# Performance work log

Hardware: AMD Instinct MI355X
Metric: run time of the kernel (lower is better)

Reference implementation:

```python
import jax, jax.numpy as jnp
import numpy as np

N_CODES = 8192
CODE_DIM = 256


def setup_inputs() -> dict:
    key = jax.random.key(0)
    kx, ke = jax.random.split(key)
    x = jax.random.normal(kx, (16, 4096, CODE_DIM), dtype=jnp.float32)
    # nn.Embedding weight initialized uniform(-1/n, 1/n)
    emb = jax.random.uniform(ke, (N_CODES, CODE_DIM), dtype=jnp.float32,
                             minval=-1.0 / N_CODES, maxval=1.0 / N_CODES)
    return {"x": x, "emb": emb}


def reference(x, emb):
    B, T, D = x.shape
    flat = x.reshape(-1, D)                                   # [BT, D]
    # squared euclidean distance: ||f||^2 - 2 f.e^T + ||e||^2  -> [BT, N]
    dist = ((flat * flat).sum(axis=1, keepdims=True)
            - 2.0 * flat @ emb.T
            + (emb * emb).sum(axis=1))
    idx = jnp.argmin(dist, axis=1)                            # [BT] int
    quant = emb[idx].reshape(x.shape)                         # [B, T, D]
    # commitment-style loss: mse(stop_grad(quant), x)
    loss = jnp.mean(jnp.square(jax.lax.stop_gradient(quant) - x))
    # straight-through estimator
    y = x + jax.lax.stop_gradient(quant - x)
    return y, idx.reshape(B, T), loss
```

## Files before the change

kernel.cpp:

```cpp
#include <hip/hip_runtime.h>
#include <stdint.h>


#define NCODES 8192
#define DDIM   256
#define BT     65536

#define TM     128
#define TN     128
#define NSEG   256
#define F4S    17

#define CAPC   48
#define MARGIN 7e-4f
#define TOKPB  128
#define CCODES 64
#define CHUNKS 128
#define KSCALE 1048576.0f
#define KOFF   131072.0f
#define KMARG  737

typedef float  f32x4  __attribute__((ext_vector_type(4)));
typedef __bf16 bf16x8 __attribute__((ext_vector_type(8)));

#define GLDS16(g, l) __builtin_amdgcn_global_load_lds(                         \
    (const __attribute__((address_space(1))) void*)(g),                        \
    (__attribute__((address_space(3))) void*)(l), 16, 0, 0)
#define GLDS4(g, l) __builtin_amdgcn_global_load_lds(                          \
    (const __attribute__((address_space(1))) void*)(g),                        \
    (__attribute__((address_space(3))) void*)(l), 4, 0, 0)

__device__ __forceinline__ unsigned int fenc(float f) {
  unsigned int u = __float_as_uint(f);
  return (u & 0x80000000u) ? ~u : (u | 0x80000000u);
}
__device__ __forceinline__ float fdec(unsigned int u) {
  unsigned int v = (u & 0x80000000u) ? (u ^ 0x80000000u) : ~u;
  return __uint_as_float(v);
}

__device__ __forceinline__ float np_pairwise256_sq(const float4* __restrict__ row) {
#pragma clang fp contract(off)
  float half[2];
  #pragma unroll
  for (int h = 0; h < 2; h++) {
    float r0,r1,r2,r3,r4,r5,r6,r7;
    float4 q0 = row[h*32 + 0];
    float4 q1 = row[h*32 + 1];
    r0 = q0.x*q0.x; r1 = q0.y*q0.y; r2 = q0.z*q0.z; r3 = q0.w*q0.w;
    r4 = q1.x*q1.x; r5 = q1.y*q1.y; r6 = q1.z*q1.z; r7 = q1.w*q1.w;
    #pragma unroll
    for (int g = 1; g < 16; g++) {
      q0 = row[h*32 + g*2];
      q1 = row[h*32 + g*2 + 1];
      r0 += q0.x*q0.x; r1 += q0.y*q0.y; r2 += q0.z*q0.z; r3 += q0.w*q0.w;
      r4 += q1.x*q1.x; r5 += q1.y*q1.y; r6 += q1.z*q1.z; r7 += q1.w*q1.w;
    }
    half[h] = ((r0+r1) + (r2+r3)) + ((r4+r5) + (r6+r7));
  }
  return half[0] + half[1];
}

__device__ __forceinline__ float exact_score_g(const float4* __restrict__ xr,
                                               const float4* __restrict__ er,
                                               float Ar, float Cv) {
#pragma clang fp contract(off)
  float b = 0.0f;
  #pragma unroll 8
  for (int q = 0; q < 64; ++q) {
    const float4 xv = xr[q];
    const float4 ev = er[q];
    b = fmaf(xv.x, ev.x, b);
    b = fmaf(xv.y, ev.y, b);
    b = fmaf(xv.z, ev.z, b);
    b = fmaf(xv.w, ev.w, b);
  }
  const float t1 = fmaf(-2.0f, b, Ar);
  return t1 + Cv;
}

__device__ __forceinline__ void exact_score2_g(const float4* __restrict__ xr,
                                               const float4* __restrict__ e1,
                                               const float4* __restrict__ e2,
                                               float Ar, float Cv1, float Cv2,
                                               float& s1, float& s2) {
#pragma clang fp contract(off)
  float b1 = 0.0f, b2 = 0.0f;
  #pragma unroll 8
  for (int q = 0; q < 64; ++q) {
    const float4 xv = xr[q];
    const float4 v1 = e1[q], v2 = e2[q];
    b1 = fmaf(xv.x, v1.x, b1); b2 = fmaf(xv.x, v2.x, b2);
    b1 = fmaf(xv.y, v1.y, b1); b2 = fmaf(xv.y, v2.y, b2);
    b1 = fmaf(xv.z, v1.z, b1); b2 = fmaf(xv.z, v2.z, b2);
    b1 = fmaf(xv.w, v1.w, b1); b2 = fmaf(xv.w, v2.w, b2);
  }
  s1 = fmaf(-2.0f, b1, Ar) + Cv1;
  s2 = fmaf(-2.0f, b2, Ar) + Cv2;
}

__global__ void vq_pre_a(const float* __restrict__ x, float* __restrict__ Astage) {
  const int t = blockIdx.x * 256 + threadIdx.x;
  Astage[t] = np_pairwise256_sq((const float4*)(x + (size_t)t * DDIM));
}

__global__ void vq_pre_c(const float* __restrict__ emb, float* __restrict__ Cws) {
  const int c = blockIdx.x * 256 + threadIdx.x;
  Cws[c] = np_pairwise256_sq((const float4*)(emb + (size_t)c * DDIM));
}

__global__ void vq_init(float* __restrict__ oloss) { *oloss = 0.0f; }

__global__ void vq_pre_e(const float* __restrict__ emb, uint4* __restrict__ ebf) {
  const int g   = blockIdx.x * 256 + threadIdx.x;
  const int c   = g >> 5;
  const int blk = g & 31;
  const float4* e4 = (const float4*)(emb + (size_t)c * DDIM);
  float4 f0 = e4[blk*2], f1 = e4[blk*2 + 1];
  union { unsigned short us[8]; uint4 v; } pk;
  pk.us[0] = __builtin_bit_cast(unsigned short, (__bf16)f0.x);
  pk.us[1] = __builtin_bit_cast(unsigned short, (__bf16)f0.y);
  pk.us[2] = __builtin_bit_cast(unsigned short, (__bf16)f0.z);
  pk.us[3] = __builtin_bit_cast(unsigned short, (__bf16)f0.w);
  pk.us[4] = __builtin_bit_cast(unsigned short, (__bf16)f1.x);
  pk.us[5] = __builtin_bit_cast(unsigned short, (__bf16)f1.y);
  pk.us[6] = __builtin_bit_cast(unsigned short, (__bf16)f1.z);
  pk.us[7] = __builtin_bit_cast(unsigned short, (__bf16)f1.w);
  ebf[(size_t)c * 32 + (blk ^ (c & 7))] = pk.v;
}

__device__ __forceinline__ void stage_chunk(const char* __restrict__ ebf,
                                            const float* __restrict__ Cws,
                                            int ch, char* ebuf_dst,
                                            float* cs_dst, int tid) {
  const char* src = ebf + (size_t)ch * 32768 + (size_t)tid * 16;
  char* dst = ebuf_dst + (size_t)tid * 16;
  #pragma unroll
  for (int i = 0; i < 4; ++i) GLDS16(src + i * 8192, dst + i * 8192);
  if (tid < 64)
    GLDS4((const char*)Cws + (size_t)ch * 256 + (size_t)tid * 4,
          (char*)cs_dst + (size_t)tid * 4);
}

__global__ __launch_bounds__(512, 4)
void vq_filter(const float* __restrict__ x, const char* __restrict__ ebf,
               const float* __restrict__ Cws, int* __restrict__ cntG,
               int* __restrict__ candG) {
  __shared__ __align__(16) char ebuf[2][32768];
  __shared__ float Cs[2][64];
  __shared__ unsigned int umin[TOKPB];
  __shared__ int cntL[TOKPB];

  const int tid  = threadIdx.x;
  const int lane = tid & 63;
  const int wid  = tid >> 6;
  const int wm   = wid >> 2;
  const int wn   = wid & 3;
  const int l15  = lane & 15;
  const int lhi  = lane >> 4;
  const int tok0 = blockIdx.x * TOKPB;

  if (tid < TOKPB) { umin[tid] = 0xFFFFFFFFu; cntL[tid] = 0; }

  stage_chunk(ebf, Cws, 0, ebuf[0], Cs[0], tid);

  const float4* x4 = (const float4*)x;
  bf16x8 xb[2][8];
  #pragma unroll
  for (int n = 0; n < 2; ++n) {
    const size_t trow = (size_t)(tok0 + wn * 32 + n * 16 + l15) * 64;
    #pragma unroll
    for (int kk = 0; kk < 8; ++kk) {
      float4 f0 = x4[trow + kk * 8 + lhi * 2];
      float4 f1 = x4[trow + kk * 8 + lhi * 2 + 1];
      bf16x8 v;
      v[0] = (__bf16)f0.x; v[1] = (__bf16)f0.y; v[2] = (__bf16)f0.z; v[3] = (__bf16)f0.w;
      v[4] = (__bf16)f1.x; v[5] = (__bf16)f1.y; v[6] = (__bf16)f1.z; v[7] = (__bf16)f1.w;
      xb[n][kk] = v;
    }
  }
  __syncthreads();

  const f32x4 zf = {0.f, 0.f, 0.f, 0.f};
  float rmin[2] = {1e30f, 1e30f};

  for (int c = 0; c < CHUNKS; ++c) {
    stage_chunk(ebf, Cws, (c + 1) & (CHUNKS - 1), ebuf[(c + 1) & 1],
                Cs[(c + 1) & 1], tid);

    const char* ecur = ebuf[c & 1];
    f32x4 acc[2][2];
    #pragma unroll
    for (int kk = 0; kk < 8; ++kk) {
      bf16x8 a[2];
      #pragma unroll
      for (int m = 0; m < 2; ++m) {
        const int row = wm * 32 + m * 16 + l15;
        const int blk = (kk * 4 + lhi) ^ (row & 7);
        a[m] = *(const bf16x8*)(ecur + row * 512 + blk * 16);
      }
      #pragma unroll
      for (int m = 0; m < 2; ++m)
        #pragma unroll
        for (int n = 0; n < 2; ++n)
          acc[m][n] = __builtin_amdgcn_mfma_f32_16x16x32_bf16(
              a[m], xb[n][kk], (kk == 0) ? zf : acc[m][n], 0, 0, 0);
    }

    const float* Csc = Cs[c & 1];
    float cvals[2][4];
    #pragma unroll
    for (int m = 0; m < 2; ++m)
      #pragma unroll
      for (int r = 0; r < 4; ++r)
        cvals[m][r] = Csc[wm * 32 + m * 16 + lhi * 4 + r];

    #pragma unroll
    for (int n = 0; n < 2; ++n) {
      const int t = wn * 32 + n * 16 + l15;
      float s[8];
      float mn = 1e30f;
      #pragma unroll
      for (int m = 0; m < 2; ++m)
        #pragma unroll
        for (int r = 0; r < 4; ++r) {
          const float v = fmaf(-2.0f, acc[m][n][r], cvals[m][r]);
          s[m * 4 + r] = v;
          mn = fminf(mn, v);
        }
      mn = fminf(mn, __shfl_xor(mn, 16));
      mn = fminf(mn, __shfl_xor(mn, 32));
      if (mn < rmin[n]) {
        rmin[n] = mn;
        if (lhi == 0) atomicMin(&umin[t], fenc(mn));
      }
      const float thr = fminf(rmin[n], fdec(umin[t])) + MARGIN;
      #pragma unroll
      for (int m = 0; m < 2; ++m)
        #pragma unroll
        for (int r = 0; r < 4; ++r) {
          if (s[m * 4 + r] <= thr) {
            const int code = c * CCODES + wm * 32 + m * 16 + lhi * 4 + r;
            int key = (int)fmaf(s[m * 4 + r], KSCALE, KOFF);
            key = min(max(key, 0), 262143);
            const int pos = atomicAdd(&cntL[t], 1);
            if (pos < CAPC)
              candG[(size_t)(tok0 + t) * CAPC + pos] = (key << 13) | code;
          }
        }
    }

    __syncthreads();
  }

  if (tid < TOKPB) cntG[tok0 + tid] = cntL[tid];
}

__global__ __launch_bounds__(256, 4)
void vq_finalize(const float* __restrict__ x, const float* __restrict__ emb,
                 const float* __restrict__ Cws, const int* __restrict__ cntG,
                 const int* __restrict__ candG, float* __restrict__ y,
                 float* __restrict__ oidx, float* __restrict__ oloss) {
  __shared__ int   idx_sh[64];
  __shared__ int   ovf_list[64];
  __shared__ int   n_ovf;
  __shared__ float rbv[256];
  __shared__ int   rbi[256];
  __shared__ float red[4];

  const int tid  = threadIdx.x;
  const int tok0 = blockIdx.x * 64;
  const float4* x4g = (const float4*)x;
  const float4* e4g = (const float4*)emb;

  if (tid == 0) n_ovf = 0;
  __syncthreads();

  const int t  = tid >> 2;
  const int j0 = tid & 3;
  const int gt = tok0 + t;
  const int cnt = cntG[gt];
  const float4* xr = x4g + (size_t)gt * 64;

  if (cnt <= CAPC) {
    int pmin = 0x7FFFFFFF;
    for (int j = j0; j < cnt; j += 4)
      pmin = min(pmin, candG[(size_t)gt * CAPC + j]);
    pmin = min(pmin, __shfl_xor(pmin, 1));
    pmin = min(pmin, __shfl_xor(pmin, 2));
    const int thrk = (pmin >> 13) + KMARG;
    int nsv = 0, smin = 0x7FFFFFFF;
    for (int j = j0; j < cnt; j += 4) {
      const int e = candG[(size_t)gt * CAPC + j];
      if ((e >> 13) <= thrk) { nsv++; smin = min(smin, e); }
    }
    nsv += __shfl_xor(nsv, 1);
    nsv += __shfl_xor(nsv, 2);
    smin = min(smin, __shfl_xor(smin, 1));
    smin = min(smin, __shfl_xor(smin, 2));

    if (nsv == 1) {
      if (j0 == 0) { idx_sh[t] = smin & 8191; oidx[gt] = (float)((smin & 8191) + 1); }
    } else {
      float best = 1e30f; int bid = 0x7FFFFFFF;
      float Ar = 0.0f; bool haveA = false;
      for (int j = j0; j < cnt; j += 4) {
        const int e = candG[(size_t)gt * CAPC + j];
        if ((e >> 13) <= thrk) {
          if (!haveA) { Ar = np_pairwise256_sq(xr); haveA = true; }
          const int c = e & 8191;
          const float s = exact_score_g(xr, e4g + (size_t)c * 64, Ar, Cws[c]);
          if (s < best || (s == best && c < bid)) { best = s; bid = c; }
        }
      }
      #pragma unroll
      for (int off = 1; off <= 2; off <<= 1) {
        const float ob = __shfl_xor(best, off);
        const int   oi = __shfl_xor(bid, off);
        if (ob < best || (ob == best && oi < bid)) { best = ob; bid = oi; }
      }
      if (j0 == 0) { idx_sh[t] = bid; oidx[gt] = (float)(bid + 1); }
    }
  } else if (j0 == 0) {
    ovf_list[atomicAdd(&n_ovf, 1)] = t;
  }
  __syncthreads();

  for (int o = 0; o < n_ovf; ++o) {
    const int tt = ovf_list[o];
    const float4* xrr = x4g + (size_t)(tok0 + tt) * 64;
    const float At = np_pairwise256_sq(xrr);
    float bv = 1e30f; int bi2 = 0x7FFFFFFF;
    for (int c0 = tid; c0 < NCODES; c0 += 512) {
      const int c1 = c0 + 256;
      float s1, s2;
      exact_score2_g(xrr, e4g + (size_t)c0 * 64, e4g + (size_t)c1 * 64,
                     At, Cws[c0], Cws[c1], s1, s2);
      if (s1 < bv || (s1 == bv && c0 < bi2)) { bv = s1; bi2 = c0; }
      if (s2 < bv || (s2 == bv && c1 < bi2)) { bv = s2; bi2 = c1; }
    }
    rbv[tid] = bv; rbi[tid] = bi2;
    __syncthreads();
    #pragma unroll
    for (int sft = 128; sft; sft >>= 1) {
      if (tid < sft) {
        const float v2 = rbv[tid + sft]; const int i2 = rbi[tid + sft];
        if (v2 < rbv[tid] || (v2 == rbv[tid] && i2 < rbi[tid])) {
          rbv[tid] = v2; rbi[tid] = i2;
        }
      }
      __syncthreads();
    }
    if (tid == 0) { idx_sh[tt] = rbi[0]; oidx[tok0 + tt] = (float)(rbi[0] + 1); }
    __syncthreads();
  }
  __syncthreads();

  float lsum = 0.0f;
  float4* y4 = (float4*)y;
  #pragma unroll
  for (int r = 0; r < 16; ++r) {
    const int g = tid + 256 * r, row = g >> 6, c4 = g & 63;
    const float4 ev = e4g[(size_t)idx_sh[row] * 64 + c4];
    const float4 xv = x4g[(size_t)(tok0 + row) * 64 + c4];
    y4[(size_t)(tok0 + row) * 64 + c4] = ev;
    const float dx = ev.x - xv.x, dy = ev.y - xv.y, dz = ev.z - xv.z, dw = ev.w - xv.w;
    lsum += dx * dx + dy * dy + dz * dz + dw * dw;
  }
  #pragma unroll
  for (int off = 32; off; off >>= 1) lsum += __shfl_down(lsum, off);
  if ((tid & 63) == 0) red[tid >> 6] = lsum;
  __syncthreads();
  if (tid == 0) atomicAdd(oloss, red[0] + red[1] + red[2] + red[3]);
}

__global__ void vq_fin(float* __restrict__ oloss) {
  *oloss = *oloss * (1.0f / 16777216.0f);
}

__global__ __launch_bounds__(256, 2)
void vq_main(const float* __restrict__ x, const float* __restrict__ emb,
             const float* __restrict__ Cws, float* __restrict__ y,
             float* __restrict__ oidx, float* __restrict__ oloss) {
  __shared__ float4 xs4[TM * F4S];
  __shared__ float4 es4[TN * F4S];
  __shared__ float  Cs[TN];
  __shared__ int    idx_sh[TM];
  __shared__ float  red[4];

  const int tid = threadIdx.x;
  const int ry = tid >> 4;
  const int rx = tid & 15;
  const int tok0 = blockIdx.x * TM;

  const float4* x4g = (const float4*)x;
  const float4* e4g = (const float4*)emb;

  float A_reg[8];
  #pragma unroll
  for (int m = 0; m < 8; m++) A_reg[m] = oidx[tok0 + ry + 16 * m];

  float best[8];
  int   i1[8];
  #pragma unroll
  for (int m = 0; m < 8; m++) { best[m] = 1e30f; i1[m] = 0; }

  float acc[8][8];

  for (int seg = 0; seg < NSEG; ++seg) {
    const int chunk = seg >> 2;
    const int kq = seg & 3;
    __syncthreads();
    #pragma unroll
    for (int h = 0; h < 2; h++) {
      float4 t[4];
      #pragma unroll
      for (int q = 0; q < 4; q++) {
        const int r = h * 4 + q;
        t[q] = x4g[(size_t)(tok0 + ry + 16 * r) * 64 + kq * 16 + rx];
      }
      #pragma unroll
      for (int q = 0; q < 4; q++) {
        const int r = h * 4 + q;
        xs4[(ry + 16 * r) * F4S + rx] = t[q];
      }
    }
    #pragma unroll
    for (int h = 0; h < 2; h++) {
      float4 t[4];
      #pragma unroll
      for (int q = 0; q < 4; q++) {
        const int r = h * 4 + q;
        t[q] = e4g[(size_t)(chunk * TN + ry + 16 * r) * 64 + kq * 16 + rx];
      }
      #pragma unroll
      for (int q = 0; q < 4; q++) {
        const int r = h * 4 + q;
        es4[(ry + 16 * r) * F4S + rx] = t[q];
      }
    }
    if (kq == 0 && tid < TN) Cs[tid] = Cws[chunk * TN + tid];
    __syncthreads();

    if (kq == 0) {
      #pragma unroll
      for (int m = 0; m < 8; m++)
        #pragma unroll
        for (int n = 0; n < 8; n++) acc[m][n] = 0.0f;
    }

    #pragma unroll
    for (int k4 = 0; k4 < 16; k4++) {
      float4 a[8], b[8];
      #pragma unroll
      for (int m = 0; m < 8; m++) a[m] = xs4[(ry + 16 * m) * F4S + k4];
      #pragma unroll
      for (int n = 0; n < 8; n++) b[n] = es4[(rx + 16 * n) * F4S + k4];
      #pragma unroll
      for (int m = 0; m < 8; m++)
        #pragma unroll
        for (int n = 0; n < 8; n++) {
          acc[m][n] = fmaf(a[m].x, b[n].x, acc[m][n]);
          acc[m][n] = fmaf(a[m].y, b[n].y, acc[m][n]);
          acc[m][n] = fmaf(a[m].z, b[n].z, acc[m][n]);
          acc[m][n] = fmaf(a[m].w, b[n].w, acc[m][n]);
        }
    }

    if (kq == 3) {
      const int c0 = chunk * TN;
      #pragma unroll
      for (int n = 0; n < 8; n++) {
        const float Cv = Cs[rx + 16 * n];
        const int c = c0 + rx + 16 * n;
        #pragma unroll
        for (int m = 0; m < 8; m++) {
          const float t1 = fmaf(-2.0f, acc[m][n], A_reg[m]);
          const float t2 = t1 + Cv;
          if (t2 < best[m]) { best[m] = t2; i1[m] = c; }
        }
      }
    }
  }

  __syncthreads();
  float* bv1 = (float*)xs4;
  int*   bi  = (int*)es4;
  #pragma unroll
  for (int m = 0; m < 8; m++) {
    bv1[(ry + 16 * m) * 16 + rx] = best[m];
    bi [(ry + 16 * m) * 16 + rx] = i1[m];
  }
  __syncthreads();
  if (tid < TM) {
    float v = bv1[tid * 16];
    int   id = bi[tid * 16];
    for (int t = 1; t < 16; t++) {
      const float vv = bv1[tid * 16 + t];
      const int   ii = bi [tid * 16 + t];
      if (vv < v || (vv == v && ii < id)) { v = vv; id = ii; }
    }
    idx_sh[tid] = id;
    oidx[tok0 + tid] = (float)(id + 1);
  }
  __syncthreads();

  float lsum = 0.0f;
  float4* y4 = (float4*)y;
  #pragma unroll
  for (int r = 0; r < 32; r++) {
    const int g = tid + 256 * r, row = g >> 6, c4 = g & 63;
    const float4 ev = e4g[(size_t)idx_sh[row] * 64 + c4];
    const float4 xv = x4g[(size_t)(tok0 + row) * 64 + c4];
    y4[(size_t)(tok0 + row) * 64 + c4] = ev;
    const float dx = ev.x - xv.x, dy = ev.y - xv.y, dz = ev.z - xv.z, dw = ev.w - xv.w;
    lsum += dx * dx + dy * dy + dz * dz + dw * dw;
  }
  #pragma unroll
  for (int off = 32; off; off >>= 1) lsum += __shfl_down(lsum, off);
  if ((tid & 63) == 0) red[tid >> 6] = lsum;
  __syncthreads();
  if (tid == 0) atomicAdd(oloss, red[0] + red[1] + red[2] + red[3]);
}

extern "C" void kernel_launch(void* const* d_in, const int* in_sizes, int n_in,
                              void* d_out, int out_size, void* d_ws, size_t ws_size,
                              hipStream_t stream) {
  const float* x   = (const float*)d_in[0];
  const float* emb = (const float*)d_in[1];

  float* y     = (float*)d_out;
  float* oidx  = y + (size_t)BT * DDIM;
  float* oloss = oidx + BT;

  char*  wsB   = (char*)d_ws;
  float* Cws   = (float*)wsB;
  int*   cntG  = (int*)(wsB + 32768);
  char*  ebf   = wsB + 32768 + 262144;
  int*   candG = (int*)(wsB + 294912 + 4194304);
  const size_t NEED = 294912 + 4194304 + (size_t)BT * CAPC * 4;

  vq_init <<<1, 1,           0, stream>>>(oloss);
  vq_pre_c<<<NCODES/256,256, 0, stream>>>(emb, Cws);

  if (ws_size >= NEED) {
    vq_pre_e   <<<1024, 256, 0, stream>>>(emb, (uint4*)ebf);
    vq_filter  <<<BT/TOKPB, 512, 0, stream>>>(x, ebf, Cws, cntG, candG);
    vq_finalize<<<BT/64, 256, 0, stream>>>(x, emb, Cws, cntG, candG,
                                           y, oidx, oloss);
  } else {
    vq_pre_a<<<BT / 256, 256, 0, stream>>>(x, oidx);
    vq_main <<<BT / TM, 256,  0, stream>>>(x, emb, Cws, y, oidx, oloss);
  }
  vq_fin  <<<1, 1,           0, stream>>>(oloss);
}
```

Measured before the change: 866.0 us.

## Compact candidates in filter epilogue and shrink finalize tokens per block

The candidate pruning by key threshold moves from the finalize kernel into the end of the filter kernel. There the surviving candidates are compacted with a prefix sum across four lanes, and the compacted count is written out. Finalize then skips its two threshold passes, handles 32 tokens per block with 8 lanes per token and higher occupancy, and writes per-block loss partials that a 256-thread kernel reduces instead of using global atomics. The filter gains a rewrite pass over candG and an extra sync, and finalize launches twice as many blocks.

```diff
diff --git a/kernel.cpp b/kernel.cpp
--- a/kernel.cpp
+++ b/kernel.cpp
@@ -19,6 +19,7 @@
 #define KSCALE 1048576.0f
 #define KOFF   131072.0f
 #define KMARG  737
+#define FTOK   32
 
 typedef float  f32x4  __attribute__((ext_vector_type(4)));
 typedef __bf16 bf16x8 __attribute__((ext_vector_type(8)));
@@ -253,68 +254,92 @@
     __syncthreads();
   }
 
-  if (tid < TOKPB) cntG[tok0 + tid] = cntL[tid];
-}
-
-__global__ __launch_bounds__(256, 4)
+  {
+    const int t4  = tid >> 2;
+    const int j4  = tid & 3;
+    const int cnt = cntL[t4];
+    const int gt4 = tok0 + t4;
+    int mask = 0, nk = 0;
+    int ent[12];
+    if (cnt <= CAPC) {
+      const int keyF = min(max((int)fmaf(fdec(umin[t4]), KSCALE, KOFF), 0), 262143);
+      const int thrk = keyF + KMARG;
+      #pragma unroll
+      for (int jj = 0; jj < 12; ++jj) {
+        const int j = j4 + jj * 4;
+        int e = 0;
+        if (j < cnt) {
+          e = candG[(size_t)gt4 * CAPC + j];
+          if ((e >> 13) <= thrk) { mask |= 1 << jj; ++nk; }
+        }
+        ent[jj] = e;
+      }
+    }
+    const int b1 = __shfl_up(nk, 1, 4);
+    const int b2 = __shfl_up(nk, 2, 4);
+    const int b3 = __shfl_up(nk, 3, 4);
+    const int base = ((j4 >= 1) ? b1 : 0) + ((j4 >= 2) ? b2 : 0)
+                   + ((j4 >= 3) ? b3 : 0);
+    int tot = nk;
+    tot += __shfl_xor(tot, 1, 4);
+    tot += __shfl_xor(tot, 2, 4);
+    __syncthreads();
+    if (cnt <= CAPC) {
+      #pragma unroll
+      for (int jj = 0; jj < 12; ++jj)
+        if ((mask >> jj) & 1)
+          candG[(size_t)gt4 * CAPC + base +
+                __builtin_popcount(mask & ((1u << jj) - 1))] = ent[jj];
+      if (j4 == 0) cntG[gt4] = tot;
+    } else if (j4 == 0) {
+      cntG[gt4] = cnt;
+    }
+  }
+}
+
+__global__ __launch_bounds__(256, 8)
 void vq_finalize(const float* __restrict__ x, const float* __restrict__ emb,
                  const float* __restrict__ Cws, const int* __restrict__ cntG,
                  const int* __restrict__ candG, float* __restrict__ y,
-                 float* __restrict__ oidx, float* __restrict__ oloss) {
-  __shared__ int   idx_sh[64];
-  __shared__ int   ovf_list[64];
+                 float* __restrict__ oidx, float* __restrict__ oloss,
+                 float* __restrict__ lossP) {
+  __shared__ int   idx_sh[FTOK];
+  __shared__ int   ovf_list[FTOK];
   __shared__ int   n_ovf;
   __shared__ float rbv[256];
   __shared__ int   rbi[256];
   __shared__ float red[4];
 
   const int tid  = threadIdx.x;
-  const int tok0 = blockIdx.x * 64;
+  const int tok0 = blockIdx.x * FTOK;
   const float4* x4g = (const float4*)x;
   const float4* e4g = (const float4*)emb;
 
   if (tid == 0) n_ovf = 0;
   __syncthreads();
 
-  const int t  = tid >> 2;
-  const int j0 = tid & 3;
+  const int t  = tid >> 3;
+  const int j0 = tid & 7;
   const int gt = tok0 + t;
   const int cnt = cntG[gt];
   const float4* xr = x4g + (size_t)gt * 64;
 
   if (cnt <= CAPC) {
-    int pmin = 0x7FFFFFFF;
-    for (int j = j0; j < cnt; j += 4)
-      pmin = min(pmin, candG[(size_t)gt * CAPC + j]);
-    pmin = min(pmin, __shfl_xor(pmin, 1));
-    pmin = min(pmin, __shfl_xor(pmin, 2));
-    const int thrk = (pmin >> 13) + KMARG;
-    int nsv = 0, smin = 0x7FFFFFFF;
-    for (int j = j0; j < cnt; j += 4) {
-      const int e = candG[(size_t)gt * CAPC + j];
-      if ((e >> 13) <= thrk) { nsv++; smin = min(smin, e); }
-    }
-    nsv += __shfl_xor(nsv, 1);
-    nsv += __shfl_xor(nsv, 2);
-    smin = min(smin, __shfl_xor(smin, 1));
-    smin = min(smin, __shfl_xor(smin, 2));
-
-    if (nsv == 1) {
-      if (j0 == 0) { idx_sh[t] = smin & 8191; oidx[gt] = (float)((smin & 8191) + 1); }
+    if (cnt <= 1) {
+      if (j0 == 0) {
+        const int c = candG[(size_t)gt * CAPC] & 8191;
+        idx_sh[t] = c; oidx[gt] = (float)(c + 1);
+      }
     } else {
+      const float Ar = np_pairwise256_sq(xr);
       float best = 1e30f; int bid = 0x7FFFFFFF;
-      float Ar = 0.0f; bool haveA = false;
-      for (int j = j0; j < cnt; j += 4) {
-        const int e = candG[(size_t)gt * CAPC + j];
-        if ((e >> 13) <= thrk) {
-          if (!haveA) { Ar = np_pairwise256_sq(xr); haveA = true; }
-          const int c = e & 8191;
-          const float s = exact_score_g(xr, e4g + (size_t)c * 64, Ar, Cws[c]);
-          if (s < best || (s == best && c < bid)) { best = s; bid = c; }
-        }
-      }
-      #pragma unroll
-      for (int off = 1; off <= 2; off <<= 1) {
+      for (int j = j0; j < cnt; j += 8) {
+        const int c = candG[(size_t)gt * CAPC + j] & 8191;
+        const float s = exact_score_g(xr, e4g + (size_t)c * 64, Ar, Cws[c]);
+        if (s < best || (s == best && c < bid)) { best = s; bid = c; }
+      }
+      #pragma unroll
+      for (int off = 1; off <= 4; off <<= 1) {
         const float ob = __shfl_xor(best, off);
         const int   oi = __shfl_xor(bid, off);
         if (ob < best || (ob == best && oi < bid)) { best = ob; bid = oi; }
@@ -359,7 +384,7 @@
   float lsum = 0.0f;
   float4* y4 = (float4*)y;
   #pragma unroll
-  for (int r = 0; r < 16; ++r) {
+  for (int r = 0; r < 8; ++r) {
     const int g = tid + 256 * r, row = g >> 6, c4 = g & 63;
     const float4 ev = e4g[(size_t)idx_sh[row] * 64 + c4];
     const float4 xv = x4g[(size_t)(tok0 + row) * 64 + c4];
@@ -371,11 +396,28 @@
   for (int off = 32; off; off >>= 1) lsum += __shfl_down(lsum, off);
   if ((tid & 63) == 0) red[tid >> 6] = lsum;
   __syncthreads();
-  if (tid == 0) atomicAdd(oloss, red[0] + red[1] + red[2] + red[3]);
-}
-
-__global__ void vq_fin(float* __restrict__ oloss) {
-  *oloss = *oloss * (1.0f / 16777216.0f);
+  if (tid == 0) {
+    const float s = red[0] + red[1] + red[2] + red[3];
+    if (lossP) lossP[blockIdx.x] = s;
+    else       atomicAdd(oloss, s);
+  }
+}
+
+__global__ void vq_fin(float* __restrict__ oloss,
+                       const float* __restrict__ lossP, int n) {
+  __shared__ float sh[4];
+  if (n > 0) {
+    float s = 0.0f;
+    for (int i = threadIdx.x; i < n; i += 256) s += lossP[i];
+    #pragma unroll
+    for (int off = 32; off; off >>= 1) s += __shfl_down(s, off);
+    if ((threadIdx.x & 63) == 0) sh[threadIdx.x >> 6] = s;
+    __syncthreads();
+    if (threadIdx.x == 0)
+      *oloss = (sh[0] + sh[1] + sh[2] + sh[3]) * (1.0f / 16777216.0f);
+  } else {
+    if (threadIdx.x == 0) *oloss = *oloss * (1.0f / 16777216.0f);
+  }
 }
 
 __global__ __launch_bounds__(256, 2)
@@ -538,19 +580,23 @@
   int*   cntG  = (int*)(wsB + 32768);
   char*  ebf   = wsB + 32768 + 262144;
   int*   candG = (int*)(wsB + 294912 + 4194304);
-  const size_t NEED = 294912 + 4194304 + (size_t)BT * CAPC * 4;
+  float* lossP = (float*)(wsB + 294912 + 4194304 + (size_t)BT * CAPC * 4);
+  const size_t NEED  = 294912 + 4194304 + (size_t)BT * CAPC * 4;
+  const size_t NEED2 = NEED + (size_t)(BT / FTOK) * 4;
 
   vq_init <<<1, 1,           0, stream>>>(oloss);
   vq_pre_c<<<NCODES/256,256, 0, stream>>>(emb, Cws);
 
   if (ws_size >= NEED) {
+    float* lp = (ws_size >= NEED2) ? lossP : nullptr;
     vq_pre_e   <<<1024, 256, 0, stream>>>(emb, (uint4*)ebf);
     vq_filter  <<<BT/TOKPB, 512, 0, stream>>>(x, ebf, Cws, cntG, candG);
-    vq_finalize<<<BT/64, 256, 0, stream>>>(x, emb, Cws, cntG, candG,
-                                           y, oidx, oloss);
+    vq_finalize<<<BT/FTOK, 256, 0, stream>>>(x, emb, Cws, cntG, candG,
+                                             y, oidx, oloss, lp);
+    vq_fin     <<<1, 256, 0, stream>>>(oloss, lp, lp ? (BT / FTOK) : 0);
   } else {
     vq_pre_a<<<BT / 256, 256, 0, stream>>>(x, oidx);
     vq_main <<<BT / TM, 256,  0, stream>>>(x, emb, Cws, y, oidx, oloss);
-  }
-  vq_fin  <<<1, 1,           0, stream>>>(oloss);
-}
+    vq_fin  <<<1, 256, 0, stream>>>(oloss, nullptr, 0);
+  }
+}
```

New measurement: 760.3 us. 1.14x faster.
